# Optimization experiments

Hardware: AMD Instinct MI355X
Metric: run time of the kernel (lower is better)

Reference implementation:

```python
import jax, jax.numpy as jnp
import numpy as np

T, A, B_IMG, Z, READ_N, WRITE_N, ENC, DEC, BATCH = 16, 64, 64, 128, 8, 8, 512, 512, 512
EPS = 1e-8


def setup_inputs() -> dict:
    key = jax.random.key(0)
    ks = jax.random.split(key, 16)
    s = 0.05
    n = lambda k, shape: jax.random.normal(k, shape, jnp.float32) * s
    return {
        "x": jax.random.uniform(ks[0], (BATCH, B_IMG * A), jnp.float32),
        "eps": jax.random.normal(ks[1], (T, BATCH, Z), jnp.float32),
        "enc_Wih": n(ks[2], (4 * ENC, 2 * READ_N * READ_N + DEC)),
        "enc_Whh": n(ks[3], (4 * ENC, ENC)),
        "enc_b": jnp.zeros((4 * ENC,), jnp.float32),
        "mu_W": n(ks[4], (Z, ENC)),
        "mu_b": jnp.zeros((Z,), jnp.float32),
        "sig_W": n(ks[5], (Z, ENC)),
        "sig_b": jnp.zeros((Z,), jnp.float32),
        "dec_Wih": n(ks[6], (4 * DEC, Z)),
        "dec_Whh": n(ks[7], (4 * DEC, DEC)),
        "dec_b": jnp.zeros((4 * DEC,), jnp.float32),
        "write_W": n(ks[8], (WRITE_N * WRITE_N, DEC)),
        "write_b": jnp.zeros((WRITE_N * WRITE_N,), jnp.float32),
        "attn_W": n(ks[9], (5, DEC)),
        "attn_b": jnp.zeros((5,), jnp.float32),
    }


def _lstm(x, h, c, Wih, Whh, b):
    g = x @ Wih.T + h @ Whh.T + b  # [bs, 4H]
    i, f, gg, o = jnp.split(g, 4, axis=1)
    c2 = jax.nn.sigmoid(f) * c + jax.nn.sigmoid(i) * jnp.tanh(gg)
    return jax.nn.sigmoid(o) * jnp.tanh(c2), c2


def _filterbank(gx, gy, sigma2, delta, N):
    # gx, gy, sigma2, delta: [bs, 1]
    grid = jnp.arange(N, dtype=jnp.float32)[None, :]  # [1, N]
    mu_x = gx + (grid - 0.5 * N - 0.5) * delta  # [bs, N]
    mu_y = gy + (grid - 0.5 * N - 0.5) * delta
    a = jnp.arange(A, dtype=jnp.float32)
    b = jnp.arange(B_IMG, dtype=jnp.float32)
    s2 = sigma2[:, :, None]  # [bs,1,1]
    Fx = jnp.exp(-((a[None, None, :] - mu_x[:, :, None]) ** 2) / (2 * s2))  # [bs,N,A]
    Fx = Fx / (Fx.sum(2, keepdims=True) + EPS)
    Fy = jnp.exp(-((b[None, None, :] - mu_y[:, :, None]) ** 2) / (2 * s2))  # [bs,N,B]
    Fy = Fy / (Fy.sum(2, keepdims=True) + EPS)
    return Fx, Fy


def _attn_window(h_dec, N, attn_W, attn_b):
    p = h_dec @ attn_W.T + attn_b  # [bs,5]
    gx_, gy_, log_s2, log_d, log_g = jnp.split(p, 5, axis=1)
    gx = (A + 1) * 0.5 * (gx_ + 1)
    gy = (B_IMG + 1) * 0.5 * (gy_ + 1)
    delta = (max(A, B_IMG) - 1) * jnp.exp(log_d) / (N - 1)
    Fx, Fy = _filterbank(gx, gy, jnp.exp(log_s2), delta, N)
    return Fx, Fy, jnp.exp(log_g)  # gamma: [bs,1]


def reference(x, eps, enc_Wih, enc_Whh, enc_b, mu_W, mu_b, sig_W, sig_b,
              dec_Wih, dec_Whh, dec_b, write_W, write_b, attn_W, attn_b):
    bs = x.shape[0]
    img = x.reshape(bs, B_IMG, A)

    def step(carry, e):
        h_enc, c_enc, h_dec, c_dec, canvas = carry
        x_hat = x - jax.nn.sigmoid(canvas)
        # --- read with attention ---
        Fx, Fy, gamma = _attn_window(h_dec, READ_N, attn_W, attn_b)
        def glimpse(im):  # Fy @ im @ Fx^T -> [bs, N, N]
            g = jnp.einsum('bnh,bhw,bmw->bnm', Fy, im, Fx)
            return g.reshape(bs, READ_N * READ_N) * gamma
        r = jnp.concatenate([glimpse(img), glimpse(x_hat.reshape(bs, B_IMG, A))], axis=1)
        # --- encoder LSTM ---
        h_enc, c_enc = _lstm(jnp.concatenate([r, h_dec], 1), h_enc, c_enc, enc_Wih, enc_Whh, enc_b)
        # --- latent sample ---
        mu = h_enc @ mu_W.T + mu_b
        log_sigma = h_enc @ sig_W.T + sig_b
        z = mu + e * jnp.exp(log_sigma)
        # --- decoder LSTM ---
        h_dec, c_dec = _lstm(z, h_dec, c_dec, dec_Wih, dec_Whh, dec_b)
        # --- write with attention ---
        w = (h_dec @ write_W.T + write_b).reshape(bs, WRITE_N, WRITE_N)
        Fx2, Fy2, gamma2 = _attn_window(h_dec, WRITE_N, attn_W, attn_b)
        wr = jnp.einsum('bnh,bnm,bma->bha', Fy2, w, Fx2).reshape(bs, B_IMG * A) / gamma2
        canvas = canvas + wr
        return (h_enc, c_enc, h_dec, c_dec, canvas), canvas

    z32 = jnp.zeros((bs, ENC), jnp.float32)
    init = (z32, z32, jnp.zeros((bs, DEC), jnp.float32), jnp.zeros((bs, DEC), jnp.float32),
            jnp.zeros((bs, B_IMG * A), jnp.float32))
    _, cs = jax.lax.scan(step, init, eps)
    return cs  # [T, bs, B*A]
```

## Files before the change

kernel.cpp:

```cpp
#include <hip/hip_runtime.h>

#define LDF 68
#define EPSF 1e-8f
#define MFMA(A,B,C) __builtin_amdgcn_mfma_f32_16x16x32_bf16((A),(B),(C),0,0,0)

typedef __attribute__((ext_vector_type(8))) short bf16x8;
typedef __attribute__((ext_vector_type(4))) float f32x4;

__device__ __forceinline__ float sigf(float x){ return 1.0f/(1.0f + __expf(-x)); }

__device__ __forceinline__ unsigned short f2bf(float f){
  unsigned u = __float_as_uint(f);
  u += 0x7FFFu + ((u >> 16) & 1u);
  return (unsigned short)(u >> 16);
}
__device__ __forceinline__ float bf2f(unsigned short s){
  return __uint_as_float((unsigned)s << 16);
}

__device__ __forceinline__ size_t pk(int b, int col, int KB){
  return ((((size_t)((b>>4)*KB + (col>>5)))*64) + (size_t)((b&15) + (((col>>3)&3)<<4)))*8 + (col&7);
}

__device__ __forceinline__ void gload_lds16(const void* g, void* l){
  __builtin_amdgcn_global_load_lds(
      (const __attribute__((address_space(1))) void*)g,
      (__attribute__((address_space(3))) void*)l, 16, 0, 0);
}

__global__ void pack_w_mfma(const float* __restrict__ Wih, const float* __restrict__ Whh,
                            int K_ih, int K_tot,
                            unsigned short* __restrict__ dhi, unsigned short* __restrict__ dlo,
                            int total8){
  int idx = blockIdx.x*256 + threadIdx.x;
  if (idx >= total8) return;
  int lane = idx & 63;
  int rest = idx >> 6;
  int KB = K_tot >> 5;
  int kb = rest % KB;
  int fm = rest / KB;
  int rr = fm*16 + (lane & 15);
  int orow = (rr & 3)*512 + (rr >> 2);
  int k0 = kb*32 + (lane >> 4)*8;
  union { unsigned short s[8]; uint4 u; } vh, vl;
  #pragma unroll
  for (int i = 0; i < 8; i++){
    int k = k0 + i;
    float f = (k < K_ih) ? Wih[(size_t)orow*K_ih + k]
                         : Whh[(size_t)orow*512 + (k - K_ih)];
    unsigned short hi = f2bf(f);
    vh.s[i] = hi;
    vl.s[i] = f2bf(f - bf2f(hi));
  }
  *(uint4*)(dhi + (size_t)idx*8) = vh.u;
  *(uint4*)(dlo + (size_t)idx*8) = vl.u;
}

__global__ void init_misc(const float* __restrict__ enc_b, const float* __restrict__ dec_b,
                          const float* __restrict__ writeW,
                          const float* __restrict__ muW, const float* __restrict__ sigW,
                          float* __restrict__ bE, float* __restrict__ bD,
                          float* __restrict__ WwT,
                          unsigned short* __restrict__ Wzh, unsigned short* __restrict__ Wzl){
  int idx = blockIdx.x*256 + threadIdx.x;
  if (idx < 2048){
    bE[idx] = enc_b[(idx & 3)*512 + (idx >> 2)];
    return;
  }
  idx -= 2048;
  if (idx < 2048){
    bD[idx] = dec_b[(idx & 3)*512 + (idx >> 2)];
    return;
  }
  idx -= 2048;
  if (idx < 32768){
    int k = idx >> 6, n = idx & 63;
    WwT[idx] = writeW[n*512 + k];
    return;
  }
  idx -= 32768;
  if (idx < 16384){
    int lane = idx & 63, rest = idx >> 6;
    int kb = rest & 15, fmf = rest >> 4;
    int row = fmf*16 + (lane & 15);
    const float* src = (row < 128) ? (muW + (size_t)row*512) : (sigW + (size_t)(row-128)*512);
    int k0 = kb*32 + (lane >> 4)*8;
    union { unsigned short s[8]; uint4 u; } vh, vl;
    #pragma unroll
    for (int i = 0; i < 8; i++){
      float f = src[k0 + i];
      unsigned short hi = f2bf(f);
      vh.s[i] = hi;
      vl.s[i] = f2bf(f - bf2f(hi));
    }
    *(uint4*)(Wzh + (size_t)idx*8) = vh.u;
    *(uint4*)(Wzl + (size_t)idx*8) = vl.u;
  }
}

__global__ void zero_f(float* p, int n){
  int idx = blockIdx.x*256 + threadIdx.x;
  if (idx < n) p[idx] = 0.f;
}

template<int KB>
__global__ __launch_bounds__(512) void mfma_gemm_lstm(
    const bf16x8* __restrict__ Wh, const bf16x8* __restrict__ Wl,
    const unsigned short* __restrict__ act, int actPlane,
    const float4* __restrict__ bias4, const float* __restrict__ c_in,
    float* __restrict__ h_f32, float* __restrict__ c_out,
    unsigned short* __restrict__ out0, int KB0, int off0, int plane0,
    unsigned short* __restrict__ out1, int KB1, int off1, int plane1)
{
  __shared__ __align__(16) unsigned char lds[3][8192];
  const int tid = threadIdx.x, lane = tid & 63, w = tid >> 6;
  const int mt = blockIdx.x & 15, nt = blockIdx.x >> 4;

  const int fmg = mt*8 + w;
  const bf16x8* whp = Wh + ((size_t)fmg*KB)*64 + lane;
  const bf16x8* wlp = Wl + ((size_t)fmg*KB)*64 + lane;
  const char* ast = (const char*)act + (size_t)(w & 1)*((size_t)actPlane*2)
                  + ((size_t)(nt*4 + (w >> 1))*KB)*1024 + (size_t)lane*16;

  const int j0 = fmg*4 + (lane >> 4);
  float4 bb = bias4[j0];
  f32x4 acc[4];
  #pragma unroll
  for (int fn = 0; fn < 4; fn++){ acc[fn][0]=bb.x; acc[fn][1]=bb.y; acc[fn][2]=bb.z; acc[fn][3]=bb.w; }

  gload_lds16(ast, (char*)&lds[0][w*1024]);
  bf16x8 whA = whp[0], wlA = wlp[0];
  __builtin_amdgcn_sched_barrier(0);
  asm volatile("" ::: "memory");
  gload_lds16(ast + 1024, (char*)&lds[1][w*1024]);
  bf16x8 whB = whp[64], wlB = wlp[64];
  __builtin_amdgcn_sched_barrier(0);
  asm volatile("" ::: "memory");

  #pragma unroll
  for (int kb = 0; kb < KB; kb++){
    if (kb + 1 < KB) asm volatile("s_waitcnt vmcnt(3)" ::: "memory");
    else             asm volatile("s_waitcnt vmcnt(0)" ::: "memory");
    __builtin_amdgcn_s_barrier();
    asm volatile("" ::: "memory");
    __builtin_amdgcn_sched_barrier(0);
    bf16x8 whC = whA, wlC = wlA;
    if (kb + 2 < KB){
      gload_lds16(ast + (size_t)(kb+2)*1024, (char*)&lds[(kb+2)%3][w*1024]);
      whC = whp[(kb+2)*64]; wlC = wlp[(kb+2)*64];
    }
    const unsigned char* rb = &lds[kb%3][0] + (size_t)lane*16;
    #pragma unroll
    for (int fn = 0; fn < 4; fn++){
      bf16x8 ah = *(const bf16x8*)(rb + fn*2048);
      bf16x8 al = *(const bf16x8*)(rb + fn*2048 + 1024);
      acc[fn] = MFMA(whA, ah, acc[fn]);
      acc[fn] = MFMA(wlA, ah, acc[fn]);
      acc[fn] = MFMA(whA, al, acc[fn]);
    }
    whA = whB; wlA = wlB; whB = whC; wlB = wlC;
  }

  const int bbase = nt*64 + (lane & 15);
  #pragma unroll
  for (int fn = 0; fn < 4; fn++){
    f32x4 g = acc[fn];
    int b = bbase + fn*16;
    float ig = sigf(g[0]);
    float fg = sigf(g[1]);
    float gg = tanhf(g[2]);
    float og = sigf(g[3]);
    float c2 = fg * c_in[(size_t)b*512 + j0] + ig * gg;
    float h  = og * tanhf(c2);
    c_out[(size_t)b*512 + j0] = c2;
    if (h_f32) h_f32[(size_t)b*512 + j0] = h;
    unsigned short hh = f2bf(h);
    unsigned short hl = f2bf(h - bf2f(hh));
    size_t o0 = pk(b, off0 + j0, KB0);
    out0[o0] = hh; out0[o0 + plane0] = hl;
    if (out1){
      size_t o1 = pk(b, off1 + j0, KB1);
      out1[o1] = hh; out1[o1 + plane1] = hl;
    }
  }
}

__global__ __launch_bounds__(512) void zgemm8(
    const unsigned short* __restrict__ Wzh, const unsigned short* __restrict__ Wzl,
    const unsigned short* __restrict__ az, int planeZ,
    const float* __restrict__ mu_b, const float* __restrict__ sig_b,
    const float* __restrict__ eps_t,
    unsigned short* __restrict__ actD, int planeD)
{
  __shared__ float zred[8*64*8];
  const int tid = threadIdx.x, lane = tid & 63, w = tid >> 6;
  const int fmb = blockIdx.x & 7, cg = blockIdx.x >> 3;
  const char* azh = (const char*)az + (size_t)cg*16384 + (size_t)lane*16;
  const char* azl = (const char*)(az + planeZ) + (size_t)cg*16384 + (size_t)lane*16;
  const int kb0 = w*2;

  bf16x8 a0h = *(const bf16x8*)(azh + (size_t)kb0*1024);
  bf16x8 a0l = *(const bf16x8*)(azl + (size_t)kb0*1024);
  bf16x8 a1h = *(const bf16x8*)(azh + (size_t)(kb0+1)*1024);
  bf16x8 a1l = *(const bf16x8*)(azl + (size_t)(kb0+1)*1024);

  const bf16x8* wmh = (const bf16x8*)Wzh + (size_t)(fmb    *16)*64 + lane;
  const bf16x8* wml = (const bf16x8*)Wzl + (size_t)(fmb    *16)*64 + lane;
  const bf16x8* wsh = (const bf16x8*)Wzh + (size_t)((fmb+8)*16)*64 + lane;
  const bf16x8* wsl = (const bf16x8*)Wzl + (size_t)((fmb+8)*16)*64 + lane;
  bf16x8 m0h = wmh[kb0*64],     m0l = wml[kb0*64];
  bf16x8 s0h = wsh[kb0*64],     s0l = wsl[kb0*64];
  bf16x8 m1h = wmh[(kb0+1)*64], m1l = wml[(kb0+1)*64];
  bf16x8 s1h = wsh[(kb0+1)*64], s1l = wsl[(kb0+1)*64];

  f32x4 am = {0.f,0.f,0.f,0.f}, as = {0.f,0.f,0.f,0.f};
  am = MFMA(m0h,a0h,am); am = MFMA(m0l,a0h,am); am = MFMA(m0h,a0l,am);
  as = MFMA(s0h,a0h,as); as = MFMA(s0l,a0h,as); as = MFMA(s0h,a0l,as);
  am = MFMA(m1h,a1h,am); am = MFMA(m1l,a1h,am); am = MFMA(m1h,a1l,am);
  as = MFMA(s1h,a1h,as); as = MFMA(s1l,a1h,as); as = MFMA(s1h,a1l,as);

  *(f32x4*)&zred[(size_t)(w*64+lane)*8]     = am;
  *(f32x4*)&zred[(size_t)(w*64+lane)*8 + 4] = as;
  __syncthreads();

  if (w == 0){
    const int r0 = fmb*16 + (lane >> 4)*4;
    float4 bm = *(const float4*)&mu_b[r0];
    float4 bs = *(const float4*)&sig_b[r0];
    f32x4 AM = {bm.x,bm.y,bm.z,bm.w};
    f32x4 AS = {bs.x,bs.y,bs.z,bs.w};
    #pragma unroll
    for (int v = 0; v < 8; v++){
      AM += *(f32x4*)&zred[(size_t)(v*64+lane)*8];
      AS += *(f32x4*)&zred[(size_t)(v*64+lane)*8 + 4];
    }
    const int b = cg*16 + (lane & 15);
    float4 ev = *(const float4*)&eps_t[(size_t)b*128 + r0];
    float e[4] = {ev.x, ev.y, ev.z, ev.w};
    union { unsigned short s[4]; uint2 u; } zh, zl;
    #pragma unroll
    for (int i = 0; i < 4; i++){
      float z = AM[i] + e[i]*__expf(AS[i]);
      unsigned short hi = f2bf(z);
      zh.s[i] = hi;
      zl.s[i] = f2bf(z - bf2f(hi));
    }
    size_t o = pk(b, r0, 20);
    *(uint2*)(actD + o) = zh.u;
    *(uint2*)(actD + planeD + o) = zl.u;
  }
}

__device__ void attn_window(const float* __restrict__ h,
                            const float* __restrict__ attn_W,
                            const float* __restrict__ attn_b,
                            float* Fx, float* Fy, float* pl)
{
  int tid = threadIdx.x;
  int lane = tid & 63, wid = tid >> 6;
  for (int q = wid; q < 5; q += 4){
    float s = 0.f;
    for (int k = lane; k < 512; k += 64) s += h[k]*attn_W[q*512 + k];
    for (int m = 32; m; m >>= 1) s += __shfl_xor(s, m);
    if (lane == 0) pl[q] = s + attn_b[q];
  }
  __syncthreads();
  float gx    = 32.5f*(pl[0] + 1.f);
  float gy    = 32.5f*(pl[1] + 1.f);
  float s2    = __expf(pl[2]);
  float delta = 9.f*__expf(pl[3]);
  float inv2  = 1.f/(2.f*s2);
  int n = tid >> 5, a = tid & 31;
  float mux = gx + ((float)n - 4.5f)*delta;
  float muy = gy + ((float)n - 4.5f)*delta;
  float dx0 = (float)a      - mux, dx1 = (float)(a+32) - mux;
  float dy0 = (float)a      - muy, dy1 = (float)(a+32) - muy;
  float e0 = __expf(-dx0*dx0*inv2), e1 = __expf(-dx1*dx1*inv2);
  float f0 = __expf(-dy0*dy0*inv2), f1 = __expf(-dy1*dy1*inv2);
  float sx = e0 + e1, sy = f0 + f1;
  for (int m = 16; m; m >>= 1){ sx += __shfl_xor(sx, m); sy += __shfl_xor(sy, m); }
  float rx = 1.f/(sx + EPSF), ry = 1.f/(sy + EPSF);
  Fx[n*LDF + a]      = e0*rx;  Fx[n*LDF + a + 32] = e1*rx;
  Fy[n*LDF + a]      = f0*ry;  Fy[n*LDF + a + 32] = f1*ry;
  __syncthreads();
}

__global__ __launch_bounds__(256) void wg_kernel(
    const float* __restrict__ h_dec,
    const float* __restrict__ WwT, const float* __restrict__ write_b,
    const float* __restrict__ attn_W, const float* __restrict__ attn_b,
    const float* __restrict__ canvas_prev, float* __restrict__ canvas_out,
    const float* __restrict__ x,
    unsigned short* __restrict__ rout, int planeE)
{
  __shared__ float hs[512];
  __shared__ float Fx[8*LDF], Fy[8*LDF], pl[8];
  __shared__ float cs[64*LDF];
  __shared__ float img_s[64*LDF];
  __shared__ float P[2][8*LDF];
  __shared__ float ps[4][64], w_s[64];
  __shared__ float tmp[64*8];
  const int b = blockIdx.x, tid = threadIdx.x;

  for (int i = tid; i < 128; i += 256)
    ((float4*)hs)[i] = ((const float4*)(h_dec + (size_t)b*512))[i];
  if (rout){
    const float4* x4 = (const float4*)(x + (size_t)b*4096);
    for (int i = tid; i < 1024; i += 256){
      int row = i >> 4, cb = (i & 15)*4;
      *(float4*)&img_s[row*LDF + cb] = x4[i];
    }
  }
  __syncthreads();
  attn_window(hs, attn_W, attn_b, Fx, Fy, pl);
  float gamma = __expf(pl[4]);

  if (canvas_out){
    {
      int j = tid & 63, part = tid >> 6;
      float s = 0.f;
      int kb = part*128;
      for (int k = 0; k < 128; k++) s += hs[kb + k] * WwT[(kb + k)*64 + j];
      ps[part][j] = s;
    }
    __syncthreads();
    if (tid < 64)
      w_s[tid] = write_b[tid] + ps[0][tid] + ps[1][tid] + ps[2][tid] + ps[3][tid];
    __syncthreads();
    float inv_g = __expf(-pl[4]);
    #pragma unroll
    for (int e = 0; e < 2; e++){
      int gi = e*256 + tid;
      int m = gi & 7, hh = gi >> 3;
      float s = 0.f;
      #pragma unroll
      for (int nn = 0; nn < 8; nn++) s += Fy[nn*LDF + hh] * w_s[nn*8 + m];
      tmp[hh*8 + m] = s;
    }
    __syncthreads();
    for (int e = 0; e < 16; e++){
      int idx = e*256 + tid;
      int hh = idx >> 6, a = idx & 63;
      float s = 0.f;
      #pragma unroll
      for (int m = 0; m < 8; m++) s += tmp[hh*8 + m] * Fx[m*LDF + a];
      float prev = canvas_prev ? canvas_prev[(size_t)b*4096 + idx] : 0.f;
      float cv = prev + s*inv_g;
      canvas_out[(size_t)b*4096 + idx] = cv;
      cs[hh*LDF + a] = cv;
    }
  } else {
    for (int e = 0; e < 16; e++){
      int idx = e*256 + tid;
      cs[(idx >> 6)*LDF + (idx & 63)] = 0.f;
    }
  }
  if (!rout) return;
  __syncthreads();
  for (int e = 0; e < 16; e++){
    int idx = e*256 + tid;
    int hh = idx >> 6, a = idx & 63;
    cs[hh*LDF + a] = sigf(cs[hh*LDF + a]);
  }
  __syncthreads();
  #pragma unroll
  for (int e = 0; e < 4; e++){
    int gi = e*256 + tid;
    int d = gi >> 9, rem = gi & 511;
    int m = rem & 7, hh = rem >> 3;
    const float* S = d ? cs : img_s;
    float s = 0.f;
    #pragma unroll
    for (int w4 = 0; w4 < 64; w4 += 4){
      float4 iv = *(const float4*)&S[hh*LDF + w4];
      float4 fv = *(const float4*)&Fx[m*LDF + w4];
      s += iv.x*fv.x + iv.y*fv.y + iv.z*fv.z + iv.w*fv.w;
    }
    P[d][m*LDF + hh] = s;
  }
  __syncthreads();
  if (tid < 128){
    int d = tid >> 6, l = tid & 63;
    int n = l >> 3, m = l & 7;
    float s = 0.f;
    #pragma unroll
    for (int h4 = 0; h4 < 64; h4 += 4){
      float4 fv = *(const float4*)&Fy[n*LDF + h4];
      float4 pv = *(const float4*)&P[d][m*LDF + h4];
      s += fv.x*pv.x + fv.y*pv.y + fv.z*pv.z + fv.w*pv.w;
    }
    tmp[d*64 + l] = s;
  }
  __syncthreads();
  if (tid < 64){
    float g1 = tmp[tid]*gamma;
    float g2 = (tmp[tid] - tmp[64 + tid])*gamma;
    unsigned short h1 = f2bf(g1), l1 = f2bf(g1 - bf2f(h1));
    unsigned short h2 = f2bf(g2), l2 = f2bf(g2 - bf2f(h2));
    size_t o1 = pk(b, tid, 36);
    size_t o2 = pk(b, 64 + tid, 36);
    rout[o1] = h1; rout[o1 + planeE] = l1;
    rout[o2] = h2; rout[o2 + planeE] = l2;
  }
}

extern "C" void kernel_launch(void* const* d_in, const int* in_sizes, int n_in,
                              void* d_out, int out_size, void* d_ws, size_t ws_size,
                              hipStream_t stream)
{
  (void)in_sizes; (void)n_in; (void)out_size; (void)ws_size;
  const float* x       = (const float*)d_in[0];
  const float* eps     = (const float*)d_in[1];
  const float* encWih  = (const float*)d_in[2];
  const float* encWhh  = (const float*)d_in[3];
  const float* enc_b   = (const float*)d_in[4];
  const float* muW     = (const float*)d_in[5];
  const float* mu_b    = (const float*)d_in[6];
  const float* sigW    = (const float*)d_in[7];
  const float* sig_b   = (const float*)d_in[8];
  const float* decWih  = (const float*)d_in[9];
  const float* decWhh  = (const float*)d_in[10];
  const float* dec_b   = (const float*)d_in[11];
  const float* writeW  = (const float*)d_in[12];
  const float* write_b = (const float*)d_in[13];
  const float* attnW   = (const float*)d_in[14];
  const float* attn_b  = (const float*)d_in[15];
  float* out = (float*)d_out;

  char* p = (char*)d_ws;
  auto alloc = [&](size_t bytes){ char* r = p; p += (bytes + 255) & ~(size_t)255; return r; };

  const int KE = 1152, KD = 640;
  const int PE = 512*KE, PD = 512*KD, PZ = 512*512;
  const int T8E = 128*36*64, T8D = 128*20*64;

  unsigned short* WpEh = (unsigned short*)alloc((size_t)T8E*16);
  unsigned short* WpEl = (unsigned short*)alloc((size_t)T8E*16);
  unsigned short* WpDh = (unsigned short*)alloc((size_t)T8D*16);
  unsigned short* WpDl = (unsigned short*)alloc((size_t)T8D*16);
  unsigned short* Wzh  = (unsigned short*)alloc(16384*16);
  unsigned short* Wzl  = (unsigned short*)alloc(16384*16);
  float* bE  = (float*)alloc(2048*4);
  float* bD  = (float*)alloc(2048*4);
  float* WwT = (float*)alloc(512*64*4);
  char* z0 = p;
  unsigned short* actE0 = (unsigned short*)alloc((size_t)2*PE*2);
  unsigned short* actD0 = (unsigned short*)alloc((size_t)2*PD*2);
  float* hDf = (float*)alloc(512*512*4);
  float* cE0 = (float*)alloc(512*512*4);
  float* cD0 = (float*)alloc(512*512*4);
  size_t zbytes = (size_t)(p - z0);
  unsigned short* actE1 = (unsigned short*)alloc((size_t)2*PE*2);
  unsigned short* actD1 = (unsigned short*)alloc((size_t)2*PD*2);
  unsigned short* AZ    = (unsigned short*)alloc((size_t)2*PZ*2);
  float* cE1 = (float*)alloc(512*512*4);
  float* cD1 = (float*)alloc(512*512*4);

  unsigned short* actE[2] = { actE0, actE1 };
  unsigned short* actD[2] = { actD0, actD1 };
  float* cEf[2] = { cE0, cE1 };
  float* cDf[2] = { cD0, cD1 };

  int tot;
  tot = T8E;   pack_w_mfma<<<(tot+255)/256,256,0,stream>>>(encWih, encWhh, 640, KE, WpEh, WpEl, tot);
  tot = T8D;   pack_w_mfma<<<(tot+255)/256,256,0,stream>>>(decWih, decWhh, 128, KD, WpDh, WpDl, tot);
  tot = 2048+2048+32768+16384;
  init_misc<<<(tot+255)/256,256,0,stream>>>(enc_b, dec_b, writeW, muW, sigW,
                                            bE, bD, WwT, Wzh, Wzl);
  tot = (int)(zbytes/4); zero_f<<<(tot+255)/256,256,0,stream>>>((float*)z0, tot);

  wg_kernel<<<512,256,0,stream>>>(hDf, WwT, write_b, attnW, attn_b,
                                  nullptr, nullptr, x, actE[0], PE);

  for (int t = 0; t < 16; t++){
    int cur = t & 1, nxt = cur ^ 1;

    mfma_gemm_lstm<36><<<128,512,0,stream>>>(
        (const bf16x8*)WpEh, (const bf16x8*)WpEl, actE[cur], PE,
        (const float4*)bE, cEf[cur], nullptr, cEf[nxt],
        AZ, 16, 0, PZ,
        actE[nxt], 36, 640, PE);

    zgemm8<<<256,512,0,stream>>>(
        Wzh, Wzl, AZ, PZ, mu_b, sig_b,
        eps + (size_t)t*65536, actD[cur], PD);

    mfma_gemm_lstm<20><<<128,512,0,stream>>>(
        (const bf16x8*)WpDh, (const bf16x8*)WpDl, actD[cur], PD,
        (const float4*)bD, cDf[cur], hDf, cDf[nxt],
        actE[nxt], 36, 128, PE,
        actD[nxt], 20, 128, PD);

    wg_kernel<<<512,256,0,stream>>>(hDf, WwT, write_b, attnW, attn_b,
                                    t ? (out + (size_t)(t-1)*2097152) : nullptr,
                                    out + (size_t)t*2097152, x,
                                    (t < 15) ? actE[nxt] : nullptr, PE);
  }
}
```

Measured before the change: 995.9 us.

## Split LSTM GEMM work across 256 blocks with two N-tiles per wave

Each wave in the fused LSTM GEMM kernel now computes 2 of the 4 batch sub-tiles instead of all 4, and the M tiling doubles to 32 tiles so the grid grows from 128 to 256 blocks. The goal is more workgroups across the GPU's compute units and two independent interleaved MFMA accumulator chains per wave. In exchange, each weight fragment is loaded by twice as many waves, which raises global weight traffic, and each wave issues fewer MFMAs per load.

```diff
diff --git a/kernel.cpp b/kernel.cpp
--- a/kernel.cpp
+++ b/kernel.cpp
@@ -114,19 +114,18 @@
 {
   __shared__ __align__(16) unsigned char lds[3][8192];
   const int tid = threadIdx.x, lane = tid & 63, w = tid >> 6;
-  const int mt = blockIdx.x & 15, nt = blockIdx.x >> 4;
-
-  const int fmg = mt*8 + w;
-  const bf16x8* whp = Wh + ((size_t)fmg*KB)*64 + lane;
-  const bf16x8* wlp = Wl + ((size_t)fmg*KB)*64 + lane;
+  const int mt = blockIdx.x & 31, nt = blockIdx.x >> 5;
+  const int fm = w & 3, fn0 = (w >> 2) << 1;
+
+  const bf16x8* whp = Wh + ((size_t)(mt*4+fm)*KB)*64 + lane;
+  const bf16x8* wlp = Wl + ((size_t)(mt*4+fm)*KB)*64 + lane;
   const char* ast = (const char*)act + (size_t)(w & 1)*((size_t)actPlane*2)
                   + ((size_t)(nt*4 + (w >> 1))*KB)*1024 + (size_t)lane*16;
 
-  const int j0 = fmg*4 + (lane >> 4);
+  const int j0 = (mt*4+fm)*4 + (lane >> 4);
   float4 bb = bias4[j0];
-  f32x4 acc[4];
-  #pragma unroll
-  for (int fn = 0; fn < 4; fn++){ acc[fn][0]=bb.x; acc[fn][1]=bb.y; acc[fn][2]=bb.z; acc[fn][3]=bb.w; }
+  f32x4 acc0 = {bb.x, bb.y, bb.z, bb.w};
+  f32x4 acc1 = acc0;
 
   gload_lds16(ast, (char*)&lds[0][w*1024]);
   bf16x8 whA = whp[0], wlA = wlp[0];
@@ -136,6 +135,8 @@
   bf16x8 whB = whp[64], wlB = wlp[64];
   __builtin_amdgcn_sched_barrier(0);
   asm volatile("" ::: "memory");
+
+  const size_t rdoff = (size_t)fn0*2048 + (size_t)lane*16;
 
   #pragma unroll
   for (int kb = 0; kb < KB; kb++){
@@ -149,23 +150,25 @@
       gload_lds16(ast + (size_t)(kb+2)*1024, (char*)&lds[(kb+2)%3][w*1024]);
       whC = whp[(kb+2)*64]; wlC = wlp[(kb+2)*64];
     }
-    const unsigned char* rb = &lds[kb%3][0] + (size_t)lane*16;
-    #pragma unroll
-    for (int fn = 0; fn < 4; fn++){
-      bf16x8 ah = *(const bf16x8*)(rb + fn*2048);
-      bf16x8 al = *(const bf16x8*)(rb + fn*2048 + 1024);
-      acc[fn] = MFMA(whA, ah, acc[fn]);
-      acc[fn] = MFMA(wlA, ah, acc[fn]);
-      acc[fn] = MFMA(whA, al, acc[fn]);
-    }
+    const unsigned char* rb = &lds[kb%3][0] + rdoff;
+    bf16x8 a0h = *(const bf16x8*)(rb);
+    bf16x8 a0l = *(const bf16x8*)(rb + 1024);
+    bf16x8 a1h = *(const bf16x8*)(rb + 2048);
+    bf16x8 a1l = *(const bf16x8*)(rb + 3072);
+    acc0 = MFMA(whA, a0h, acc0);
+    acc1 = MFMA(whA, a1h, acc1);
+    acc0 = MFMA(wlA, a0h, acc0);
+    acc1 = MFMA(wlA, a1h, acc1);
+    acc0 = MFMA(whA, a0l, acc0);
+    acc1 = MFMA(whA, a1l, acc1);
     whA = whB; wlA = wlB; whB = whC; wlB = wlC;
   }
 
-  const int bbase = nt*64 + (lane & 15);
+  const int bb0 = nt*64 + fn0*16 + (lane & 15);
   #pragma unroll
-  for (int fn = 0; fn < 4; fn++){
-    f32x4 g = acc[fn];
-    int b = bbase + fn*16;
+  for (int n = 0; n < 2; n++){
+    f32x4 g = n ? acc1 : acc0;
+    int b = bb0 + n*16;
     float ig = sigf(g[0]);
     float fg = sigf(g[1]);
     float gg = tanhf(g[2]);
@@ -475,7 +478,7 @@
   for (int t = 0; t < 16; t++){
     int cur = t & 1, nxt = cur ^ 1;
 
-    mfma_gemm_lstm<36><<<128,512,0,stream>>>(
+    mfma_gemm_lstm<36><<<256,512,0,stream>>>(
         (const bf16x8*)WpEh, (const bf16x8*)WpEl, actE[cur], PE,
         (const float4*)bE, cEf[cur], nullptr, cEf[nxt],
         AZ, 16, 0, PZ,
@@ -485,7 +488,7 @@
         Wzh, Wzl, AZ, PZ, mu_b, sig_b,
         eps + (size_t)t*65536, actD[cur], PD);
 
-    mfma_gemm_lstm<20><<<128,512,0,stream>>>(
+    mfma_gemm_lstm<20><<<256,512,0,stream>>>(
         (const bf16x8*)WpDh, (const bf16x8*)WpDl, actD[cur], PD,
         (const float4*)bD, cDf[cur], hDf, cDf[nxt],
         actE[nxt], 36, 128, PE,
```

New measurement: 881.6 us, median of 2. -11.5%, faster.
